# Kernel tuning notes

Measured on AMD Instinct MI355X. Metric: run time of the kernel, lower is better.

The kernel has to match this reference:

```python
import jax, jax.numpy as jnp
import numpy as np

D = 1024
H = 16
HD = D // H


def setup_inputs() -> dict:
    key = jax.random.key(0)
    ks = jax.random.split(key, 9)
    s = 1.0 / np.sqrt(D)
    inp = {
        "x": jax.random.normal(ks[0], (2, 2048, D), dtype=jnp.float32),
        "Wq": jax.random.uniform(ks[1], (D, D), jnp.float32, -s, s),
        "bq": jax.random.uniform(ks[2], (D,), jnp.float32, -s, s),
        "Wk": jax.random.uniform(ks[3], (D, D), jnp.float32, -s, s),
        "bk": jax.random.uniform(ks[4], (D,), jnp.float32, -s, s),
        "Wv": jax.random.uniform(ks[5], (D, D), jnp.float32, -s, s),
        "bv": jax.random.uniform(ks[6], (D,), jnp.float32, -s, s),
        "Wo": jax.random.uniform(ks[7], (D, D), jnp.float32, -s, s),
        "bo": jax.random.uniform(ks[8], (D,), jnp.float32, -s, s),
    }
    return inp


def reference(x, Wq, bq, Wk, bk, Wv, bv, Wo, bo):
    B, S, _ = x.shape
    scale = jnp.sqrt(jnp.asarray(HD, dtype=jnp.float32))
    # QKV projections, split into heads: [B, H, S, HD]
    def proj(W, b):
        y = jnp.einsum('bsd,de->bse', x, W) + b
        return y.reshape(B, S, H, HD).transpose(0, 2, 1, 3)
    Q, K, V = proj(Wq, bq), proj(Wk, bk), proj(Wv, bv)
    scores = jnp.einsum('bhqd,bhkd->bhqk', Q, K) / scale  # [B,H,S,S]
    attn = jax.nn.softmax(scores, axis=-1)
    ctx = jnp.einsum('bhqk,bhkd->bhqd', attn, V)
    ctx = ctx.transpose(0, 2, 1, 3).reshape(B, S, D)
    return jnp.einsum('bsd,de->bse', ctx, Wo) + bo
```

## Files before the change

kernel.cpp:

```cpp
#include <hip/hip_runtime.h>
#include <hip/hip_bf16.h>

typedef __attribute__((ext_vector_type(8))) short bf16x8;
typedef __attribute__((ext_vector_type(4))) float f32x4;

constexpr int Sc  = 2048;
constexpr int Dc  = 1024;
constexpr int Hc  = 16;
constexpr int HDc = 64;
constexpr int Mc  = 4096;

constexpr float ECs = 0.18033688011112042f;

__device__ __forceinline__ ushort f2bf(float f) {
  unsigned u = __float_as_uint(f);
  u += 0x7fffu + ((u >> 16) & 1u);
  return (ushort)(u >> 16);
}
__device__ __forceinline__ float bf2f(ushort h) {
  return __uint_as_float(((unsigned)h) << 16);
}

union US8 {
  ushort u[8];
  uint   w[4];
  bf16x8 v;
};

__global__ __launch_bounds__(256) void split_x_kernel(
    const float* __restrict__ X, ushort* __restrict__ H) {
  const int i    = blockIdx.x * 256 + threadIdx.x;
  const float4 v = ((const float4*)X)[i];
  ushort4 h;
  h.x = f2bf(v.x);
  h.y = f2bf(v.y);
  h.z = f2bf(v.z);
  h.w = f2bf(v.w);
  ((ushort4*)H)[i] = h;
}

struct SplitP {
  const float* W[4];
  ushort*      Th[4];
  ushort*      Tl[4];
};

__global__ __launch_bounds__(256) void split_wt_kernel(SplitP p) {
  __shared__ float T[64][69];
  const int z = blockIdx.z;
  const float* W = p.W[z];
  const int t  = threadIdx.x;
  const int c  = (t & 15) * 4;
  const int r  = t >> 4;
  const int n0 = blockIdx.x * 64, k0 = blockIdx.y * 64;
#pragma unroll
  for (int pp = 0; pp < 4; ++pp) {
    const int k    = r + pp * 16;
    const float4 v = *(const float4*)(W + (size_t)(k0 + k) * 1024 + n0 + c);
    T[k][c + 0] = v.x;
    T[k][c + 1] = v.y;
    T[k][c + 2] = v.z;
    T[k][c + 3] = v.w;
  }
  __syncthreads();
#pragma unroll
  for (int pp = 0; pp < 4; ++pp) {
    const int n = r + pp * 16;
    const float x0 = T[c + 0][n], x1 = T[c + 1][n], x2 = T[c + 2][n], x3 = T[c + 3][n];
    ushort4 h, l;
    h.x = f2bf(x0); l.x = f2bf(x0 - bf2f(h.x));
    h.y = f2bf(x1); l.y = f2bf(x1 - bf2f(h.y));
    h.z = f2bf(x2); l.z = f2bf(x2 - bf2f(h.z));
    h.w = f2bf(x3); l.w = f2bf(x3 - bf2f(h.w));
    *(ushort4*)(p.Th[z] + (size_t)(n0 + n) * 1024 + k0 + c) = h;
    if (z != 3)
      *(ushort4*)(p.Tl[z] + (size_t)(n0 + n) * 1024 + k0 + c) = l;
  }
}

struct GemmP {
  const ushort* Bh[3];
  const ushort* Bl[3];
  const float*  bias[3];
  void*         Out[3];
};

template <bool QKV>
__global__ __launch_bounds__(256) void gemm_bf16(
    const ushort* __restrict__ A, GemmP p) {
  __shared__ __align__(16) ushort As[128 * 32];
  __shared__ __align__(16) ushort BsH[128 * 32];
  __shared__ __align__(16) ushort BsL[QKV ? 128 * 32 : 16];

  const int t  = threadIdx.x;
  const int z  = blockIdx.z;
  const int m0 = blockIdx.x * 128, n0 = blockIdx.y * 128;
  const ushort* Bh  = p.Bh[z];
  const ushort* Bl  = p.Bl[z];
  const float* bias = p.bias[z];

  const int lane = t & 63, wave = t >> 6;
  const int wm = (wave & 1) * 64, wn = (wave >> 1) * 64;

  f32x4 acc[4][4];
#pragma unroll
  for (int i = 0; i < 4; ++i)
#pragma unroll
    for (int j = 0; j < 4; ++j) acc[i][j] = (f32x4){0.f, 0.f, 0.f, 0.f};

  const int am = t >> 2;
  const int ac = t & 3;
  const ushort* gA  = A  + (size_t)(m0 + am) * 1024 + ac * 8;
  const ushort* gBh = Bh + (size_t)(n0 + am) * 1024 + ac * 8;
  const ushort* gBl = Bl + (size_t)(n0 + am) * 1024 + ac * 8;
  const int sw = ((ac + (am >> 1)) & 3) * 8;
  const int l0 = am * 32 + sw, l1 = (am + 64) * 32 + sw;

  const int fr  = lane & 15;
  const int fkb = (((lane >> 4) + (fr >> 1)) & 3) * 16;

  bf16x8 rA0, rA1, rH0, rH1, rL0, rL1;
  rA0 = *(const bf16x8*)(gA);
  rA1 = *(const bf16x8*)(gA + 64 * 1024);
  rH0 = *(const bf16x8*)(gBh);
  rH1 = *(const bf16x8*)(gBh + 64 * 1024);
  if (QKV) {
    rL0 = *(const bf16x8*)(gBl);
    rL1 = *(const bf16x8*)(gBl + 64 * 1024);
  }

  for (int k0 = 0; k0 < 1024; k0 += 32) {
    __syncthreads();
    *(bf16x8*)&As[l0]  = rA0;
    *(bf16x8*)&As[l1]  = rA1;
    *(bf16x8*)&BsH[l0] = rH0;
    *(bf16x8*)&BsH[l1] = rH1;
    if (QKV) {
      *(bf16x8*)&BsL[l0] = rL0;
      *(bf16x8*)&BsL[l1] = rL1;
    }
    __syncthreads();

    if (k0 + 32 < 1024) {
      const int kn = k0 + 32;
      rA0 = *(const bf16x8*)(gA + kn);
      rA1 = *(const bf16x8*)(gA + kn + 64 * 1024);
      rH0 = *(const bf16x8*)(gBh + kn);
      rH1 = *(const bf16x8*)(gBh + kn + 64 * 1024);
      if (QKV) {
        rL0 = *(const bf16x8*)(gBl + kn);
        rL1 = *(const bf16x8*)(gBl + kn + 64 * 1024);
      }
    }

    bf16x8 a[4], b_h[4], b_l[4];
#pragma unroll
    for (int i = 0; i < 4; ++i) {
      const int ra = (wm + i * 16 + fr) * 64 + fkb;
      const int rb = (wn + i * 16 + fr) * 64 + fkb;
      a[i]   = *(const bf16x8*)((const char*)As + ra);
      b_h[i] = *(const bf16x8*)((const char*)BsH + rb);
      if (QKV) b_l[i] = *(const bf16x8*)((const char*)BsL + rb);
    }
#pragma unroll
    for (int i = 0; i < 4; ++i)
#pragma unroll
      for (int j = 0; j < 4; ++j) {
        acc[i][j] = __builtin_amdgcn_mfma_f32_16x16x32_bf16(a[i], b_h[j], acc[i][j], 0, 0, 0);
        if (QKV)
          acc[i][j] = __builtin_amdgcn_mfma_f32_16x16x32_bf16(a[i], b_l[j], acc[i][j], 0, 0, 0);
      }
  }

  const float osc = (QKV && z == 0) ? ECs : 1.0f;
  const int cr = (lane >> 4) * 4;
  const int cc = lane & 15;
#pragma unroll
  for (int j = 0; j < 4; ++j) {
    const int n    = n0 + wn + j * 16 + cc;
    const float bv = bias[n];
#pragma unroll
    for (int i = 0; i < 4; ++i) {
      const int mb = m0 + wm + i * 16 + cr;
#pragma unroll
      for (int r = 0; r < 4; ++r) {
        const int m   = mb + r;
        const float v = (acc[i][j][r] + bv) * osc;
        if (QKV) {
          const int b = m >> 11, s = m & 2047, h = n >> 6, hd = n & 63;
          ((ushort*)p.Out[z])[(((size_t)(b * Hc + h) * Sc + s) << 6) + hd] = f2bf(v);
        } else {
          ((float*)p.Out[z])[(size_t)m * 1024 + n] = v;
        }
      }
    }
  }
}

__global__ __launch_bounds__(256) void attn_mfma3(
    const ushort* __restrict__ Q, const ushort* __restrict__ K,
    const ushort* __restrict__ V, ushort* __restrict__ CTX) {
  __shared__ __align__(16) ushort Ks[64 * 72];
  __shared__ __align__(16) ushort Vt[64 * 72];

  const int t    = threadIdx.x;
  const int lane = t & 63, wave = t >> 6;
  const int c16 = lane & 15, quad = lane >> 4;
  const int bh = blockIdx.x, qt = blockIdx.y;
  const int bb = bh >> 4, hh = bh & 15;

  const ushort* Qb = Q + (size_t)bh * Sc * HDc + (size_t)qt * 128 * HDc;
  const ushort* Kb = K + (size_t)bh * Sc * HDc;
  const ushort* Vb = V + (size_t)bh * Sc * HDc;

  bf16x8 aq[2][2];
#pragma unroll
  for (int mt = 0; mt < 2; ++mt)
#pragma unroll
    for (int c = 0; c < 2; ++c)
      aq[mt][c] = *(const bf16x8*)(Qb + (size_t)(wave * 32 + mt * 16 + c16) * 64 + c * 32 + quad * 8);

  US8 ones_u;
#pragma unroll
  for (int e = 0; e < 8; ++e) ones_u.u[e] = 0x3F80;
  const bf16x8 ones = ones_u.v;

  f32x4 ctx[2][4], lacc[2];
#pragma unroll
  for (int mt = 0; mt < 2; ++mt) {
    lacc[mt] = (f32x4){0.f, 0.f, 0.f, 0.f};
#pragma unroll
    for (int j = 0; j < 4; ++j) ctx[mt][j] = (f32x4){0.f, 0.f, 0.f, 0.f};
  }

  const int krow = t >> 2, kc = (t & 3) * 8;
  const int kg = t & 15, dg = t >> 4;
  const int lb = ((kg >> 3) << 5) | ((kg & 3) << 3) | (((kg >> 2) & 1) << 2);

  const ushort* gK = Kb + (size_t)krow * 64 + kc;
  const ushort* gV = Vb + (size_t)(kg * 4) * 64 + dg * 4;

  bf16x8 kr0, kr1;
  ushort4 vr[4];
  kr0 = *(const bf16x8*)(gK);
  kr1 = *(const bf16x8*)(gK + 32);
#pragma unroll
  for (int i = 0; i < 4; ++i) vr[i] = *(const ushort4*)(gV + (size_t)i * 64);

  for (int kt = 0; kt < 32; ++kt) {
    __syncthreads();
    *(bf16x8*)&Ks[krow * 72 + kc]      = kr0;
    *(bf16x8*)&Ks[krow * 72 + kc + 32] = kr1;
    {
      const uint* w0 = (const uint*)&vr[0];
      const uint* w1 = (const uint*)&vr[1];
      const uint* w2 = (const uint*)&vr[2];
      const uint* w3 = (const uint*)&vr[3];
#pragma unroll
      for (int j = 0; j < 4; ++j) {
        const int  wd  = j >> 1;
        const uint sel = (j & 1) ? 0x07060302u : 0x05040100u;
        const uint lo  = __builtin_amdgcn_perm(w1[wd], w0[wd], sel);
        const uint hi  = __builtin_amdgcn_perm(w3[wd], w2[wd], sel);
        *(uint2*)&Vt[(dg * 4 + j) * 72 + lb] = make_uint2(lo, hi);
      }
    }
    __syncthreads();

    if (kt < 31) {
      const size_t adv = (size_t)(kt + 1) * 64 * 64;
      kr0 = *(const bf16x8*)(gK + adv);
      kr1 = *(const bf16x8*)(gK + adv + 32);
#pragma unroll
      for (int i = 0; i < 4; ++i) vr[i] = *(const ushort4*)(gV + adv + (size_t)i * 64);
    }

    f32x4 st[2][4];
#pragma unroll
    for (int mt = 0; mt < 2; ++mt)
#pragma unroll
      for (int j = 0; j < 4; ++j) st[mt][j] = (f32x4){0.f, 0.f, 0.f, 0.f};
#pragma unroll
    for (int c = 0; c < 2; ++c)
#pragma unroll
      for (int j = 0; j < 4; ++j) {
        const bf16x8 ak = *(const bf16x8*)&Ks[(j * 16 + c16) * 72 + c * 32 + quad * 8];
        st[0][j] = __builtin_amdgcn_mfma_f32_16x16x32_bf16(ak, aq[0][c], st[0][j], 0, 0, 0);
        st[1][j] = __builtin_amdgcn_mfma_f32_16x16x32_bf16(ak, aq[1][c], st[1][j], 0, 0, 0);
      }

    US8 pf[2][2];
#pragma unroll
    for (int mt = 0; mt < 2; ++mt)
#pragma unroll
      for (int c2 = 0; c2 < 2; ++c2)
#pragma unroll
        for (int w = 0; w < 4; ++w) {
          const int jj = c2 * 2 + (w >> 1);
          const int r0 = (w & 1) * 2;
          const float pe = __builtin_amdgcn_exp2f(st[mt][jj][r0]);
          const float po = __builtin_amdgcn_exp2f(st[mt][jj][r0 + 1]);
          pf[mt][c2].w[w] = __builtin_amdgcn_perm(
              __float_as_uint(po), __float_as_uint(pe), 0x07060302u);
        }

#pragma unroll
    for (int c2 = 0; c2 < 2; ++c2) {
      lacc[0] = __builtin_amdgcn_mfma_f32_16x16x32_bf16(pf[0][c2].v, ones, lacc[0], 0, 0, 0);
      lacc[1] = __builtin_amdgcn_mfma_f32_16x16x32_bf16(pf[1][c2].v, ones, lacc[1], 0, 0, 0);
#pragma unroll
      for (int j = 0; j < 4; ++j) {
        const bf16x8 bv = *(const bf16x8*)&Vt[(j * 16 + c16) * 72 + c2 * 32 + quad * 8];
        ctx[0][j] = __builtin_amdgcn_mfma_f32_16x16x32_bf16(pf[0][c2].v, bv, ctx[0][j], 0, 0, 0);
        ctx[1][j] = __builtin_amdgcn_mfma_f32_16x16x32_bf16(pf[1][c2].v, bv, ctx[1][j], 0, 0, 0);
      }
    }
  }

#pragma unroll
  for (int mt = 0; mt < 2; ++mt) {
#pragma unroll
    for (int r = 0; r < 4; ++r) {
      const float inv = 1.f / lacc[mt][r];
      const int srow  = qt * 128 + wave * 32 + mt * 16 + quad * 4 + r;
      const size_t rb = ((size_t)(bb * Sc + srow)) * 1024 + hh * 64;
#pragma unroll
      for (int j = 0; j < 4; ++j)
        CTX[rb + j * 16 + c16] = f2bf(ctx[mt][j][r] * inv);
    }
  }
}

extern "C" void kernel_launch(void* const* d_in, const int* in_sizes, int n_in,
                              void* d_out, int out_size, void* d_ws, size_t ws_size,
                              hipStream_t stream) {
  (void)in_sizes; (void)n_in; (void)out_size; (void)ws_size;
  const float* x  = (const float*)d_in[0];
  const float* Wq = (const float*)d_in[1];
  const float* bq = (const float*)d_in[2];
  const float* Wk = (const float*)d_in[3];
  const float* bk = (const float*)d_in[4];
  const float* Wv = (const float*)d_in[5];
  const float* bv = (const float*)d_in[6];
  const float* Wo = (const float*)d_in[7];
  const float* bo = (const float*)d_in[8];

  const size_t MB = 1024 * 1024;
  char* w    = (char*)d_ws;
  ushort* Qw = (ushort*)(w + 0 * MB);
  ushort* Kw = (ushort*)(w + 8 * MB);
  ushort* Vw = (ushort*)(w + 16 * MB);
  ushort* Cw = (ushort*)(w + 24 * MB);
  ushort* Xh = (ushort*)(w + 32 * MB);
  ushort* WT = (ushort*)(w + 40 * MB);
  ushort* Whq = WT + 0 * 1048576; ushort* Wlq = WT + 1 * 1048576;
  ushort* Whk = WT + 2 * 1048576; ushort* Wlk = WT + 3 * 1048576;
  ushort* Whv = WT + 4 * 1048576; ushort* Wlv = WT + 5 * 1048576;
  ushort* Who = WT + 6 * 1048576; ushort* Wlo = WT + 7 * 1048576;

  const dim3 blk(256);

  split_x_kernel<<<4096, blk, 0, stream>>>(x, Xh);

  SplitP sp;
  sp.W[0] = Wq; sp.W[1] = Wk; sp.W[2] = Wv; sp.W[3] = Wo;
  sp.Th[0] = Whq; sp.Th[1] = Whk; sp.Th[2] = Whv; sp.Th[3] = Who;
  sp.Tl[0] = Wlq; sp.Tl[1] = Wlk; sp.Tl[2] = Wlv; sp.Tl[3] = Wlo;
  split_wt_kernel<<<dim3(16, 16, 4), blk, 0, stream>>>(sp);

  GemmP pq;
  pq.Bh[0] = Whq; pq.Bh[1] = Whk; pq.Bh[2] = Whv;
  pq.Bl[0] = Wlq; pq.Bl[1] = Wlk; pq.Bl[2] = Wlv;
  pq.bias[0] = bq; pq.bias[1] = bk; pq.bias[2] = bv;
  pq.Out[0] = Qw; pq.Out[1] = Kw; pq.Out[2] = Vw;
  gemm_bf16<true><<<dim3(Mc / 128, Dc / 128, 3), blk, 0, stream>>>(Xh, pq);

  attn_mfma3<<<dim3(2 * Hc, Sc / 128), blk, 0, stream>>>(Qw, Kw, Vw, Cw);

  GemmP po;
  po.Bh[0] = po.Bh[1] = po.Bh[2] = Who;
  po.Bl[0] = po.Bl[1] = po.Bl[2] = Wlo;
  po.bias[0] = po.bias[1] = po.bias[2] = bo;
  po.Out[0] = po.Out[1] = po.Out[2] = d_out;
  gemm_bf16<false><<<dim3(Mc / 128, Dc / 128, 1), blk, 0, stream>>>(Cw, po);
}
```

Before: 216.7 us.

## Switch pipeline from bf16 hi/lo split weights to single fp16 operands

```diff
diff --git a/kernel.cpp b/kernel.cpp
--- a/kernel.cpp
+++ b/kernel.cpp
@@ -1,7 +1,7 @@
 #include <hip/hip_runtime.h>
 #include <hip/hip_bf16.h>
 
-typedef __attribute__((ext_vector_type(8))) short bf16x8;
+typedef __attribute__((ext_vector_type(8))) _Float16 f16x8;
 typedef __attribute__((ext_vector_type(4))) float f32x4;
 
 constexpr int Sc  = 2048;
@@ -12,19 +12,14 @@
 
 constexpr float ECs = 0.18033688011112042f;
 
-__device__ __forceinline__ ushort f2bf(float f) {
-  unsigned u = __float_as_uint(f);
-  u += 0x7fffu + ((u >> 16) & 1u);
-  return (ushort)(u >> 16);
-}
-__device__ __forceinline__ float bf2f(ushort h) {
-  return __uint_as_float(((unsigned)h) << 16);
+__device__ __forceinline__ ushort f2h(float f) {
+  return __builtin_bit_cast(ushort, (_Float16)f);
 }
 
 union US8 {
   ushort u[8];
   uint   w[4];
-  bf16x8 v;
+  f16x8  v;
 };
 
 __global__ __launch_bounds__(256) void split_x_kernel(
@@ -32,17 +27,16 @@
   const int i    = blockIdx.x * 256 + threadIdx.x;
   const float4 v = ((const float4*)X)[i];
   ushort4 h;
-  h.x = f2bf(v.x);
-  h.y = f2bf(v.y);
-  h.z = f2bf(v.z);
-  h.w = f2bf(v.w);
+  h.x = f2h(v.x);
+  h.y = f2h(v.y);
+  h.z = f2h(v.z);
+  h.w = f2h(v.w);
   ((ushort4*)H)[i] = h;
 }
 
 struct SplitP {
   const float* W[4];
   ushort*      Th[4];
-  ushort*      Tl[4];
 };
 
 __global__ __launch_bounds__(256) void split_wt_kernel(SplitP p) {
@@ -66,37 +60,31 @@
 #pragma unroll
   for (int pp = 0; pp < 4; ++pp) {
     const int n = r + pp * 16;
-    const float x0 = T[c + 0][n], x1 = T[c + 1][n], x2 = T[c + 2][n], x3 = T[c + 3][n];
-    ushort4 h, l;
-    h.x = f2bf(x0); l.x = f2bf(x0 - bf2f(h.x));
-    h.y = f2bf(x1); l.y = f2bf(x1 - bf2f(h.y));
-    h.z = f2bf(x2); l.z = f2bf(x2 - bf2f(h.z));
-    h.w = f2bf(x3); l.w = f2bf(x3 - bf2f(h.w));
+    ushort4 h;
+    h.x = f2h(T[c + 0][n]);
+    h.y = f2h(T[c + 1][n]);
+    h.z = f2h(T[c + 2][n]);
+    h.w = f2h(T[c + 3][n]);
     *(ushort4*)(p.Th[z] + (size_t)(n0 + n) * 1024 + k0 + c) = h;
-    if (z != 3)
-      *(ushort4*)(p.Tl[z] + (size_t)(n0 + n) * 1024 + k0 + c) = l;
   }
 }
 
 struct GemmP {
   const ushort* Bh[3];
-  const ushort* Bl[3];
   const float*  bias[3];
   void*         Out[3];
 };
 
 template <bool QKV>
-__global__ __launch_bounds__(256) void gemm_bf16(
+__global__ __launch_bounds__(256) void gemm_f16(
     const ushort* __restrict__ A, GemmP p) {
   __shared__ __align__(16) ushort As[128 * 32];
-  __shared__ __align__(16) ushort BsH[128 * 32];
-  __shared__ __align__(16) ushort BsL[QKV ? 128 * 32 : 16];
+  __shared__ __align__(16) ushort Bs[128 * 32];
 
   const int t  = threadIdx.x;
   const int z  = blockIdx.z;
   const int m0 = blockIdx.x * 128, n0 = blockIdx.y * 128;
   const ushort* Bh  = p.Bh[z];
-  const ushort* Bl  = p.Bl[z];
   const float* bias = p.bias[z];
 
   const int lane = t & 63, wave = t >> 6;
@@ -112,64 +100,47 @@
   const int ac = t & 3;
   const ushort* gA  = A  + (size_t)(m0 + am) * 1024 + ac * 8;
   const ushort* gBh = Bh + (size_t)(n0 + am) * 1024 + ac * 8;
-  const ushort* gBl = Bl + (size_t)(n0 + am) * 1024 + ac * 8;
   const int sw = ((ac + (am >> 1)) & 3) * 8;
   const int l0 = am * 32 + sw, l1 = (am + 64) * 32 + sw;
 
   const int fr  = lane & 15;
   const int fkb = (((lane >> 4) + (fr >> 1)) & 3) * 16;
 
-  bf16x8 rA0, rA1, rH0, rH1, rL0, rL1;
-  rA0 = *(const bf16x8*)(gA);
-  rA1 = *(const bf16x8*)(gA + 64 * 1024);
-  rH0 = *(const bf16x8*)(gBh);
-  rH1 = *(const bf16x8*)(gBh + 64 * 1024);
-  if (QKV) {
-    rL0 = *(const bf16x8*)(gBl);
-    rL1 = *(const bf16x8*)(gBl + 64 * 1024);
-  }
+  f16x8 rA0, rA1, rH0, rH1;
+  rA0 = *(const f16x8*)(gA);
+  rA1 = *(const f16x8*)(gA + 64 * 1024);
+  rH0 = *(const f16x8*)(gBh);
+  rH1 = *(const f16x8*)(gBh + 64 * 1024);
 
   for (int k0 = 0; k0 < 1024; k0 += 32) {
     __syncthreads();
-    *(bf16x8*)&As[l0]  = rA0;
-    *(bf16x8*)&As[l1]  = rA1;
-    *(bf16x8*)&BsH[l0] = rH0;
-    *(bf16x8*)&BsH[l1] = rH1;
-    if (QKV) {
-      *(bf16x8*)&BsL[l0] = rL0;
-      *(bf16x8*)&BsL[l1] = rL1;
-    }
+    *(f16x8*)&As[l0] = rA0;
+    *(f16x8*)&As[l1] = rA1;
+    *(f16x8*)&Bs[l0] = rH0;
+    *(f16x8*)&Bs[l1] = rH1;
     __syncthreads();
 
     if (k0 + 32 < 1024) {
       const int kn = k0 + 32;
-      rA0 = *(const bf16x8*)(gA + kn);
-      rA1 = *(const bf16x8*)(gA + kn + 64 * 1024);
-      rH0 = *(const bf16x8*)(gBh + kn);
-      rH1 = *(const bf16x8*)(gBh + kn + 64 * 1024);
-      if (QKV) {
-        rL0 = *(const bf16x8*)(gBl + kn);
-        rL1 = *(const bf16x8*)(gBl + kn + 64 * 1024);
-      }
-    }
-
-    bf16x8 a[4], b_h[4], b_l[4];
+      rA0 = *(const f16x8*)(gA + kn);
+      rA1 = *(const f16x8*)(gA + kn + 64 * 1024);
+      rH0 = *(const f16x8*)(gBh + kn);
+      rH1 = *(const f16x8*)(gBh + kn + 64 * 1024);
+    }
+
+    f16x8 a[4], b_h[4];
 #pragma unroll
     for (int i = 0; i < 4; ++i) {
       const int ra = (wm + i * 16 + fr) * 64 + fkb;
       const int rb = (wn + i * 16 + fr) * 64 + fkb;
-      a[i]   = *(const bf16x8*)((const char*)As + ra);
-      b_h[i] = *(const bf16x8*)((const char*)BsH + rb);
-      if (QKV) b_l[i] = *(const bf16x8*)((const char*)BsL + rb);
+      a[i]   = *(const f16x8*)((const char*)As + ra);
+      b_h[i] = *(const f16x8*)((const char*)Bs + rb);
     }
 #pragma unroll
     for (int i = 0; i < 4; ++i)
 #pragma unroll
-      for (int j = 0; j < 4; ++j) {
-        acc[i][j] = __builtin_amdgcn_mfma_f32_16x16x32_bf16(a[i], b_h[j], acc[i][j], 0, 0, 0);
-        if (QKV)
-          acc[i][j] = __builtin_amdgcn_mfma_f32_16x16x32_bf16(a[i], b_l[j], acc[i][j], 0, 0, 0);
-      }
+      for (int j = 0; j < 4; ++j)
+        acc[i][j] = __builtin_amdgcn_mfma_f32_16x16x32_f16(a[i], b_h[j], acc[i][j], 0, 0, 0);
   }
 
   const float osc = (QKV && z == 0) ? ECs : 1.0f;
@@ -188,7 +159,7 @@
         const float v = (acc[i][j][r] + bv) * osc;
         if (QKV) {
           const int b = m >> 11, s = m & 2047, h = n >> 6, hd = n & 63;
-          ((ushort*)p.Out[z])[(((size_t)(b * Hc + h) * Sc + s) << 6) + hd] = f2bf(v);
+          ((ushort*)p.Out[z])[(((size_t)(b * Hc + h) * Sc + s) << 6) + hd] = f2h(v);
         } else {
           ((float*)p.Out[z])[(size_t)m * 1024 + n] = v;
         }
@@ -213,17 +184,17 @@
   const ushort* Kb = K + (size_t)bh * Sc * HDc;
   const ushort* Vb = V + (size_t)bh * Sc * HDc;
 
-  bf16x8 aq[2][2];
+  f16x8 aq[2][2];
 #pragma unroll
   for (int mt = 0; mt < 2; ++mt)
 #pragma unroll
     for (int c = 0; c < 2; ++c)
-      aq[mt][c] = *(const bf16x8*)(Qb + (size_t)(wave * 32 + mt * 16 + c16) * 64 + c * 32 + quad * 8);
+      aq[mt][c] = *(const f16x8*)(Qb + (size_t)(wave * 32 + mt * 16 + c16) * 64 + c * 32 + quad * 8);
 
   US8 ones_u;
 #pragma unroll
-  for (int e = 0; e < 8; ++e) ones_u.u[e] = 0x3F80;
-  const bf16x8 ones = ones_u.v;
+  for (int e = 0; e < 8; ++e) ones_u.u[e] = 0x3C00;
+  const f16x8 ones = ones_u.v;
 
   f32x4 ctx[2][4], lacc[2];
 #pragma unroll
@@ -240,17 +211,17 @@
   const ushort* gK = Kb + (size_t)krow * 64 + kc;
   const ushort* gV = Vb + (size_t)(kg * 4) * 64 + dg * 4;
 
-  bf16x8 kr0, kr1;
+  f16x8 kr0, kr1;
   ushort4 vr[4];
-  kr0 = *(const bf16x8*)(gK);
-  kr1 = *(const bf16x8*)(gK + 32);
+  kr0 = *(const f16x8*)(gK);
+  kr1 = *(const f16x8*)(gK + 32);
 #pragma unroll
   for (int i = 0; i < 4; ++i) vr[i] = *(const ushort4*)(gV + (size_t)i * 64);
 
   for (int kt = 0; kt < 32; ++kt) {
     __syncthreads();
-    *(bf16x8*)&Ks[krow * 72 + kc]      = kr0;
-    *(bf16x8*)&Ks[krow * 72 + kc + 32] = kr1;
+    *(f16x8*)&Ks[krow * 72 + kc]      = kr0;
+    *(f16x8*)&Ks[krow * 72 + kc + 32] = kr1;
     {
       const uint* w0 = (const uint*)&vr[0];
       const uint* w1 = (const uint*)&vr[1];
@@ -269,8 +240,8 @@
 
     if (kt < 31) {
       const size_t adv = (size_t)(kt + 1) * 64 * 64;
-      kr0 = *(const bf16x8*)(gK + adv);
-      kr1 = *(const bf16x8*)(gK + adv + 32);
+      kr0 = *(const f16x8*)(gK + adv);
+      kr1 = *(const f16x8*)(gK + adv + 32);
 #pragma unroll
       for (int i = 0; i < 4; ++i) vr[i] = *(const ushort4*)(gV + adv + (size_t)i * 64);
     }
@@ -284,9 +255,9 @@
     for (int c = 0; c < 2; ++c)
 #pragma unroll
       for (int j = 0; j < 4; ++j) {
-        const bf16x8 ak = *(const bf16x8*)&Ks[(j * 16 + c16) * 72 + c * 32 + quad * 8];
-        st[0][j] = __builtin_amdgcn_mfma_f32_16x16x32_bf16(ak, aq[0][c], st[0][j], 0, 0, 0);
-        st[1][j] = __builtin_amdgcn_mfma_f32_16x16x32_bf16(ak, aq[1][c], st[1][j], 0, 0, 0);
+        const f16x8 ak = *(const f16x8*)&Ks[(j * 16 + c16) * 72 + c * 32 + quad * 8];
+        st[0][j] = __builtin_amdgcn_mfma_f32_16x16x32_f16(ak, aq[0][c], st[0][j], 0, 0, 0);
+        st[1][j] = __builtin_amdgcn_mfma_f32_16x16x32_f16(ak, aq[1][c], st[1][j], 0, 0, 0);
       }
 
     US8 pf[2][2];
@@ -300,19 +271,19 @@
           const int r0 = (w & 1) * 2;
           const float pe = __builtin_amdgcn_exp2f(st[mt][jj][r0]);
           const float po = __builtin_amdgcn_exp2f(st[mt][jj][r0 + 1]);
-          pf[mt][c2].w[w] = __builtin_amdgcn_perm(
-              __float_as_uint(po), __float_as_uint(pe), 0x07060302u);
+          const auto pk = __builtin_amdgcn_cvt_pkrtz(pe, po);
+          pf[mt][c2].w[w] = __builtin_bit_cast(uint, pk);
         }
 
 #pragma unroll
     for (int c2 = 0; c2 < 2; ++c2) {
-      lacc[0] = __builtin_amdgcn_mfma_f32_16x16x32_bf16(pf[0][c2].v, ones, lacc[0], 0, 0, 0);
-      lacc[1] = __builtin_amdgcn_mfma_f32_16x16x32_bf16(pf[1][c2].v, ones, lacc[1], 0, 0, 0);
+      lacc[0] = __builtin_amdgcn_mfma_f32_16x16x32_f16(pf[0][c2].v, ones, lacc[0], 0, 0, 0);
+      lacc[1] = __builtin_amdgcn_mfma_f32_16x16x32_f16(pf[1][c2].v, ones, lacc[1], 0, 0, 0);
 #pragma unroll
       for (int j = 0; j < 4; ++j) {
-        const bf16x8 bv = *(const bf16x8*)&Vt[(j * 16 + c16) * 72 + c2 * 32 + quad * 8];
-        ctx[0][j] = __builtin_amdgcn_mfma_f32_16x16x32_bf16(pf[0][c2].v, bv, ctx[0][j], 0, 0, 0);
-        ctx[1][j] = __builtin_amdgcn_mfma_f32_16x16x32_bf16(pf[1][c2].v, bv, ctx[1][j], 0, 0, 0);
+        const f16x8 bv = *(const f16x8*)&Vt[(j * 16 + c16) * 72 + c2 * 32 + quad * 8];
+        ctx[0][j] = __builtin_amdgcn_mfma_f32_16x16x32_f16(pf[0][c2].v, bv, ctx[0][j], 0, 0, 0);
+        ctx[1][j] = __builtin_amdgcn_mfma_f32_16x16x32_f16(pf[1][c2].v, bv, ctx[1][j], 0, 0, 0);
       }
     }
   }
@@ -326,7 +297,7 @@
       const size_t rb = ((size_t)(bb * Sc + srow)) * 1024 + hh * 64;
 #pragma unroll
       for (int j = 0; j < 4; ++j)
-        CTX[rb + j * 16 + c16] = f2bf(ctx[mt][j][r] * inv);
+        CTX[rb + j * 16 + c16] = f2h(ctx[mt][j][r] * inv);
     }
   }
 }
@@ -353,10 +324,10 @@
   ushort* Cw = (ushort*)(w + 24 * MB);
   ushort* Xh = (ushort*)(w + 32 * MB);
   ushort* WT = (ushort*)(w + 40 * MB);
-  ushort* Whq = WT + 0 * 1048576; ushort* Wlq = WT + 1 * 1048576;
-  ushort* Whk = WT + 2 * 1048576; ushort* Wlk = WT + 3 * 1048576;
-  ushort* Whv = WT + 4 * 1048576; ushort* Wlv = WT + 5 * 1048576;
-  ushort* Who = WT + 6 * 1048576; ushort* Wlo = WT + 7 * 1048576;
+  ushort* Whq = WT + 0 * 1048576;
+  ushort* Whk = WT + 1 * 1048576;
+  ushort* Whv = WT + 2 * 1048576;
+  ushort* Who = WT + 3 * 1048576;
 
   const dim3 blk(256);
 
@@ -365,22 +336,19 @@
   SplitP sp;
   sp.W[0] = Wq; sp.W[1] = Wk; sp.W[2] = Wv; sp.W[3] = Wo;
   sp.Th[0] = Whq; sp.Th[1] = Whk; sp.Th[2] = Whv; sp.Th[3] = Who;
-  sp.Tl[0] = Wlq; sp.Tl[1] = Wlk; sp.Tl[2] = Wlv; sp.Tl[3] = Wlo;
   split_wt_kernel<<<dim3(16, 16, 4), blk, 0, stream>>>(sp);
 
   GemmP pq;
   pq.Bh[0] = Whq; pq.Bh[1] = Whk; pq.Bh[2] = Whv;
-  pq.Bl[0] = Wlq; pq.Bl[1] = Wlk; pq.Bl[2] = Wlv;
   pq.bias[0] = bq; pq.bias[1] = bk; pq.bias[2] = bv;
   pq.Out[0] = Qw; pq.Out[1] = Kw; pq.Out[2] = Vw;
-  gemm_bf16<true><<<dim3(Mc / 128, Dc / 128, 3), blk, 0, stream>>>(Xh, pq);
+  gemm_f16<true><<<dim3(Mc / 128, Dc / 128, 3), blk, 0, stream>>>(Xh, pq);
 
   attn_mfma3<<<dim3(2 * Hc, Sc / 128), blk, 0, stream>>>(Qw, Kw, Vw, Cw);
 
   GemmP po;
   po.Bh[0] = po.Bh[1] = po.Bh[2] = Who;
-  po.Bl[0] = po.Bl[1] = po.Bl[2] = Wlo;
   po.bias[0] = po.bias[1] = po.bias[2] = bo;
   po.Out[0] = po.Out[1] = po.Out[2] = d_out;
-  gemm_bf16<false><<<dim3(Mc / 128, Dc / 128, 1), blk, 0, stream>>>(Cw, po);
-}
+  gemm_f16<false><<<dim3(Mc / 128, Dc / 128, 1), blk, 0, stream>>>(Cw, po);
+}
```

Measured after the change: 199.2 us. -8.0%, faster.
